# Kernel optimization log

Hardware: AMD Instinct MI355X
Metric: run time of the kernel (lower is better)

## Reference

```python
import jax, jax.numpy as jnp
import numpy as np
import math

B, S, HID = 1, 2048, 1024
NH, NKV = 16, 4
HD = HID // NH          # 64
GROUPS = NH // NKV      # 4
ROPE_BASE = 10000.0


def setup_inputs() -> dict:
    key = jax.random.key(0)
    ks = jax.random.split(key, 5)
    hidden_states = jax.random.normal(ks[0], (B, S, HID), dtype=jnp.float32)
    # additive causal mask: 0 on/below diagonal, -1e9 above
    causal = jnp.triu(jnp.full((S, S), -1e9, dtype=jnp.float32), k=1)
    attention_mask = causal[None, None, :, :]
    position_ids = jnp.arange(S, dtype=jnp.int32)[None, :]
    sc = 0.02
    Wq = jax.random.normal(ks[1], (NH * HD, HID), dtype=jnp.float32) * sc
    Wk = jax.random.normal(ks[2], (NKV * HD, HID), dtype=jnp.float32) * sc
    Wv = jax.random.normal(ks[3], (NKV * HD, HID), dtype=jnp.float32) * sc
    Wo = jax.random.normal(ks[4], (HID, NH * HD), dtype=jnp.float32) * sc
    return {"hidden_states": hidden_states, "attention_mask": attention_mask,
            "position_ids": position_ids, "Wq": Wq, "Wk": Wk, "Wv": Wv, "Wo": Wo}


def _rotate_half(x):
    x1, x2 = jnp.split(x, 2, axis=-1)
    return jnp.concatenate([-x2, x1], axis=-1)


def _rope_cos_sin(position_ids, dtype):
    # LlamaRotaryEmbedding: inv_freq over even dims, emb = [freqs, freqs]
    inv_freq = 1.0 / (ROPE_BASE ** (jnp.arange(0, HD, 2, dtype=jnp.float32) / HD))
    freqs = position_ids.astype(jnp.float32)[..., None] * inv_freq  # [B,S,HD/2]
    emb = jnp.concatenate([freqs, freqs], axis=-1)                  # [B,S,HD]
    return jnp.cos(emb).astype(dtype)[:, None], jnp.sin(emb).astype(dtype)[:, None]


def reference(hidden_states, attention_mask, position_ids, Wq, Wk, Wv, Wo):
    b, q_len, _ = hidden_states.shape
    # torch Linear: y = x @ W.T  (W is [out, in])
    q = jnp.einsum('bsh,oh->bso', hidden_states, Wq).reshape(b, q_len, NH, HD).transpose(0, 2, 1, 3)
    k = jnp.einsum('bsh,oh->bso', hidden_states, Wk).reshape(b, q_len, NKV, HD).transpose(0, 2, 1, 3)
    v = jnp.einsum('bsh,oh->bso', hidden_states, Wv).reshape(b, q_len, NKV, HD).transpose(0, 2, 1, 3)

    cos, sin = _rope_cos_sin(position_ids, q.dtype)  # [B,1,S,HD]
    q = q * cos + _rotate_half(q) * sin
    k = k * cos + _rotate_half(k) * sin

    # repeat_kv (GQA expansion)
    k = jnp.repeat(k, GROUPS, axis=1)  # [B,NH,S,HD]
    v = jnp.repeat(v, GROUPS, axis=1)

    scores = jnp.einsum('bhqd,bhkd->bhqk', q, k) / math.sqrt(HD)
    scores = scores + attention_mask
    attn = jax.nn.softmax(scores.astype(jnp.float32), axis=-1).astype(q.dtype)
    out = jnp.einsum('bhqk,bhkd->bhqd', attn, v)
    out = out.transpose(0, 2, 1, 3).reshape(b, q_len, NH * HD)
    return jnp.einsum('bso,ho->bsh', out, Wo)
```

## Files before the change

kernel.cpp:

```cpp
#include <hip/hip_runtime.h>
#include <hip/hip_bf16.h>
#include <math.h>

#define S_LEN 2048
#define HIDN  1024
#define K_DIM 1024
#define NHEAD 16
#define NKVH  4
#define HD    64

typedef __bf16 bf16x8 __attribute__((ext_vector_type(8)));
typedef float  f32x4  __attribute__((ext_vector_type(4)));
typedef float  f32x16 __attribute__((ext_vector_type(16)));

static __device__ __forceinline__ unsigned short f2bf(float f) {
  union { float f; unsigned u; } v; v.f = f;
  unsigned u = v.u;
  u += 0x7fffu + ((u >> 16) & 1u);
  return (unsigned short)(u >> 16);
}

static __device__ __forceinline__ void gload_lds16(const unsigned short* g, unsigned short* l) {
  __builtin_amdgcn_global_load_lds((const __attribute__((address_space(1))) void*)g,
                                   (__attribute__((address_space(3))) void*)l, 16, 0, 0);
}

__global__ __launch_bounds__(256) void prep_kernel(const float* __restrict__ hs,
                                                   const float* __restrict__ Wq,
                                                   const float* __restrict__ Wk,
                                                   const float* __restrict__ Wv,
                                                   const float* __restrict__ Wo,
                                                   const int* __restrict__ pos,
                                                   unsigned short* __restrict__ hsb,
                                                   unsigned short* __restrict__ Wqkv,
                                                   unsigned short* __restrict__ Wob,
                                                   float2* __restrict__ cstab) {
  const int gid = blockIdx.x * 256 + threadIdx.x;
  if (gid < 1179648) {
    const float* src; unsigned short* dst; int i;
    if (gid < 524288)       { src = hs; dst = hsb;            i = gid; }
    else if (gid < 786432)  { src = Wq; dst = Wqkv;           i = gid - 524288; }
    else if (gid < 851968)  { src = Wk; dst = Wqkv + 1048576; i = gid - 786432; }
    else if (gid < 917504)  { src = Wv; dst = Wqkv + 1310720; i = gid - 851968; }
    else                    { src = Wo; dst = Wob;            i = gid - 917504; }
    float4 v = *(const float4*)(src + (size_t)i * 4);
    ushort4 u;
    u.x = f2bf(v.x); u.y = f2bf(v.y); u.z = f2bf(v.z); u.w = f2bf(v.w);
    *(ushort4*)(dst + (size_t)i * 4) = u;
  } else {
    int e = gid - 1179648;
    int s = e >> 5, ir = e & 31;
    float p = (float)pos[s];
    float ang = p * __expf(-(float)ir * 0.28782314f);
    float c, sn;
    sincosf(ang, &sn, &c);
    cstab[e] = make_float2(c, sn);
  }
}

template <bool ROPE>
__global__ __launch_bounds__(256, 2) void gemm_kernel(const unsigned short* __restrict__ A,
                                                      const unsigned short* __restrict__ B,
                                                      float* __restrict__ C,
                                                      const float2* __restrict__ cstab,
                                                      unsigned short* __restrict__ Qr,
                                                      unsigned short* __restrict__ Kr,
                                                      unsigned short* __restrict__ Vt) {
  __shared__ unsigned short As[2][64][64];
  __shared__ unsigned short Bs[2][128][64];
  const int m0 = blockIdx.x * 64, n0 = blockIdx.y * 128;
  const int t = threadIdx.x, w = t >> 6, lane = t & 63;
  const int lr = lane & 15, lg = lane >> 4;
  const int m_off = (w & 1) * 32, n_off = (w >> 1) * 64;
  const int rsub = lane >> 3;
  const int cole = ((lane & 7) * 8) ^ (rsub << 3);
  f32x4 acc[2][4] = {};

#define GSTAGE(b, kt) do {                                                     \
    _Pragma("unroll")                                                          \
    for (int c = 0; c < 2; ++c) {                                              \
      int ch = w * 2 + c;                                                      \
      gload_lds16(A + (size_t)(m0 + ch * 8 + rsub) * K_DIM + (kt) * 64 + cole, \
                  &As[b][0][0] + ch * 512);                                    \
    }                                                                          \
    _Pragma("unroll")                                                          \
    for (int c = 0; c < 4; ++c) {                                              \
      int ch = w * 4 + c;                                                      \
      gload_lds16(B + (size_t)(n0 + ch * 8 + rsub) * K_DIM + (kt) * 64 + cole, \
                  &Bs[b][0][0] + ch * 512);                                    \
    }                                                                          \
  } while (0)

  int cur = 0;
  GSTAGE(0, 0);
  for (int kt = 0; kt < 16; ++kt) {
    __syncthreads();
    if (kt + 1 < 16) GSTAGE(cur ^ 1, kt + 1);
#pragma unroll
    for (int kc = 0; kc < 2; ++kc) {
      bf16x8 af[2], bfg[4];
#pragma unroll
      for (int i = 0; i < 2; ++i) {
        int row = m_off + i * 16 + lr;
        af[i] = *(const bf16x8*)((const char*)&As[cur][0][0] + row * 128 +
                                 ((kc * 64 + lg * 16) ^ ((lr & 7) << 4)));
      }
#pragma unroll
      for (int jj = 0; jj < 4; ++jj) {
        int row = n_off + jj * 16 + lr;
        bfg[jj] = *(const bf16x8*)((const char*)&Bs[cur][0][0] + row * 128 +
                                   ((kc * 64 + lg * 16) ^ ((lr & 7) << 4)));
      }
#pragma unroll
      for (int i = 0; i < 2; ++i)
#pragma unroll
        for (int jj = 0; jj < 4; ++jj)
          acc[i][jj] = __builtin_amdgcn_mfma_f32_16x16x32_bf16(af[i], bfg[jj], acc[i][jj], 0, 0, 0);
    }
    cur ^= 1;
  }

  if constexpr (ROPE) {
    const int col64 = n0 + n_off;
    const int hh = col64 >> 6;
#pragma unroll
    for (int i = 0; i < 2; ++i) {
      if (hh < 20) {
#pragma unroll
        for (int r = 0; r < 4; ++r) {
          int srow = m0 + m_off + i * 16 + lg * 4 + r;
          unsigned short* dst = (hh < 16) ? (Qr + ((size_t)hh * S_LEN + srow) * HD)
                                          : (Kr + ((size_t)(hh - 16) * S_LEN + srow) * HD);
          float sc = (hh < 16) ? 0.125f : 1.0f;
#pragma unroll
          for (int jj = 0; jj < 2; ++jj) {
            int d0 = jj * 16 + lr;
            float2 cs = cstab[(size_t)srow * 32 + d0];
            float v0 = acc[i][jj][r] * sc, v1 = acc[i][jj + 2][r] * sc;
            dst[d0]      = f2bf(v0 * cs.x - v1 * cs.y);
            dst[d0 + 32] = f2bf(v1 * cs.x + v0 * cs.y);
          }
        }
      } else {
        const int khv = (col64 - 1280) >> 6;
        const int s_base = m0 + m_off + i * 16 + lg * 4;
#pragma unroll
        for (int jj = 0; jj < 4; ++jj) {
          int d = jj * 16 + lr;
          ushort4 u;
          u.x = f2bf(acc[i][jj][0]);
          u.y = f2bf(acc[i][jj][1]);
          u.z = f2bf(acc[i][jj][2]);
          u.w = f2bf(acc[i][jj][3]);
          *(ushort4*)(Vt + ((size_t)khv * HD + d) * S_LEN + s_base) = u;
        }
      }
    }
  } else {
#pragma unroll
    for (int i = 0; i < 2; ++i)
#pragma unroll
      for (int jj = 0; jj < 4; ++jj)
#pragma unroll
        for (int r = 0; r < 4; ++r)
          C[(size_t)(m0 + m_off + i * 16 + lg * 4 + r) * 1024 + n0 + n_off + jj * 16 + lr] =
              acc[i][jj][r];
  }
}

__global__ __launch_bounds__(256, 4) void attn_part(const unsigned short* __restrict__ Qr,
                                                    const unsigned short* __restrict__ Kr,
                                                    const unsigned short* __restrict__ Vt,
                                                    unsigned short* __restrict__ Ob,
                                                    float* __restrict__ Opart,
                                                    float* __restrict__ Mlpart) {
  __shared__ unsigned short Ks[2][64][64];
  __shared__ unsigned short Vs[2][64][64];
  const int bid = blockIdx.x;
  const int h = bid & 15;
  const int j = bid >> 4;
  int qt, ck;
  if (j < 16)      { qt = 15 - (j >> 2); ck = j & 3; }
  else if (j < 28) { int e = j - 16; int d3 = e / 3; qt = 11 - d3; ck = e - d3 * 3; }
  else if (j < 36) { int e = j - 28; qt = 7 - (e >> 1); ck = e & 1; }
  else             { qt = 39 - j; ck = 0; }
  const int kh = h >> 2;
  const int nkt_all = 2 * qt + 2;
  const int nch = (2 * qt + 9) >> 3;
  const int kt0 = ck * 8;
  const int kt1 = (kt0 + 8 < nkt_all) ? kt0 + 8 : nkt_all;

  const int t = threadIdx.x, w = t >> 6, lane = t & 63;
  const int ql = lane & 31, hi = lane >> 5;
  const int q = qt * 128 + w * 32 + ql;
  const int qwave_max = qt * 128 + w * 32 + 31;

  const unsigned short* Kh = Kr + (size_t)kh * S_LEN * HD;
  const unsigned short* Vh = Vt + (size_t)kh * HD * S_LEN;

  bf16x8 qf[4];
#pragma unroll
  for (int c = 0; c < 4; ++c)
    qf[c] = *(const bf16x8*)(Qr + ((size_t)h * S_LEN + q) * HD + c * 16 + hi * 8);

  const int rsub = lane >> 3;
  const int cole = ((lane & 7) * 8) ^ (rsub << 3);

#define ASTAGE(b, kt) do {                                                           \
    int k0s = (kt) * 64;                                                             \
    _Pragma("unroll")                                                                \
    for (int c = 0; c < 4; ++c) {                                                    \
      int ch = w * 4 + c;                                                            \
      if (ch < 8)                                                                    \
        gload_lds16(Kh + (size_t)(k0s + ch * 8 + rsub) * HD + cole,                  \
                    &Ks[b][0][0] + ch * 512);                                        \
      else                                                                           \
        gload_lds16(Vh + (size_t)((ch - 8) * 8 + rsub) * S_LEN + k0s + cole,         \
                    &Vs[b][0][0] + (ch - 8) * 512);                                  \
    }                                                                                \
  } while (0)

  float m_run = -1e30f, l_run = 0.f;
  f32x16 oacc[2] = {};
  int cur = 0;
  ASTAGE(0, kt0);
  for (int kt = kt0; kt < kt1; ++kt) {
    __syncthreads();
    if (kt + 1 < kt1) ASTAGE(cur ^ 1, kt + 1);
    const int k0 = kt * 64;
    if (k0 <= qwave_max) {
      f32x16 sacc[2] = {};
      __builtin_amdgcn_s_setprio(1);
#pragma unroll
      for (int tt = 0; tt < 2; ++tt)
#pragma unroll
        for (int c = 0; c < 4; ++c) {
          int row = tt * 32 + ql;
          bf16x8 kf = *(const bf16x8*)((const char*)&Ks[cur][0][0] + row * 128 +
                                       ((c * 32 + hi * 16) ^ ((ql & 7) << 4)));
          sacc[tt] = __builtin_amdgcn_mfma_f32_32x32x16_bf16(kf, qf[c], sacc[tt], 0, 0, 0);
        }
      __builtin_amdgcn_s_setprio(0);

      float p[32];
#pragma unroll
      for (int tt = 0; tt < 2; ++tt)
#pragma unroll
        for (int e = 0; e < 16; ++e) p[tt * 16 + e] = sacc[tt][e];

      if (k0 + 63 > q) {
#pragma unroll
        for (int tt = 0; tt < 2; ++tt)
#pragma unroll
          for (int e = 0; e < 16; ++e) {
            int kl = tt * 32 + (e & 3) + 8 * (e >> 2) + 4 * hi;
            if (k0 + kl > q) p[tt * 16 + e] = -1e30f;
          }
      }

      float mx = p[0];
#pragma unroll
      for (int e = 1; e < 32; ++e) mx = fmaxf(mx, p[e]);
      mx = fmaxf(mx, __shfl_xor(mx, 32));

      if (__any(mx > m_run + 8.0f)) {
        float mnew = fmaxf(m_run, mx);
        float f = __expf(m_run - mnew);
        l_run *= f;
        oacc[0] *= f; oacc[1] *= f;
        m_run = mnew;
      }

      float lsum = 0.f;
#pragma unroll
      for (int e = 0; e < 32; ++e) { p[e] = __expf(p[e] - m_run); lsum += p[e]; }
      lsum += __shfl_xor(lsum, 32);
      l_run += lsum;

      unsigned g[16];
#pragma unroll
      for (int i = 0; i < 16; ++i) {
        union { __hip_bfloat162 b; unsigned u; } cv;
        cv.b = __float22bfloat162_rn(make_float2(p[2 * i], p[2 * i + 1]));
        g[i] = cv.u;
      }
#pragma unroll
      for (int b4 = 0; b4 < 16; b4 += 8) {
        asm volatile("v_permlane32_swap_b32 %0, %1" : "+v"(g[b4 + 0]), "+v"(g[b4 + 2]));
        asm volatile("v_permlane32_swap_b32 %0, %1" : "+v"(g[b4 + 1]), "+v"(g[b4 + 3]));
        asm volatile("v_permlane32_swap_b32 %0, %1" : "+v"(g[b4 + 4]), "+v"(g[b4 + 6]));
        asm volatile("v_permlane32_swap_b32 %0, %1" : "+v"(g[b4 + 5]), "+v"(g[b4 + 7]));
      }

#pragma unroll
      for (int s = 0; s < 4; ++s) {
        union { bf16x8 v; unsigned u[4]; } pf;
        pf.u[0] = g[s * 4 + 0]; pf.u[1] = g[s * 4 + 1];
        pf.u[2] = g[s * 4 + 2]; pf.u[3] = g[s * 4 + 3];
        __builtin_amdgcn_s_setprio(1);
#pragma unroll
        for (int dt = 0; dt < 2; ++dt) {
          int row = dt * 32 + ql;
          bf16x8 vf = *(const bf16x8*)((const char*)&Vs[cur][0][0] + row * 128 +
                                       ((s * 32 + hi * 16) ^ ((ql & 7) << 4)));
          oacc[dt] = __builtin_amdgcn_mfma_f32_32x32x16_bf16(vf, pf.v, oacc[dt], 0, 0, 0);
        }
        __builtin_amdgcn_s_setprio(0);
      }
    }
    cur ^= 1;
  }

  if (nch == 1) {
    float inv = 1.f / l_run;
#pragma unroll
    for (int dt = 0; dt < 2; ++dt)
#pragma unroll
      for (int gg = 0; gg < 4; ++gg) {
        ushort4 u;
        u.x = f2bf(oacc[dt][gg * 4 + 0] * inv);
        u.y = f2bf(oacc[dt][gg * 4 + 1] * inv);
        u.z = f2bf(oacc[dt][gg * 4 + 2] * inv);
        u.w = f2bf(oacc[dt][gg * 4 + 3] * inv);
        int d0 = dt * 32 + 8 * gg + 4 * hi;
        *(ushort4*)(Ob + (size_t)q * HIDN + h * HD + d0) = u;
      }
  } else {
    const int slot = (h * 16 + qt) * 4 + ck;
    float* ob = Opart + (size_t)slot * 8192 + t * 32;
#pragma unroll
    for (int dt = 0; dt < 2; ++dt)
#pragma unroll
      for (int gg = 0; gg < 4; ++gg) {
        f32x4 v4;
        v4[0] = oacc[dt][gg * 4 + 0]; v4[1] = oacc[dt][gg * 4 + 1];
        v4[2] = oacc[dt][gg * 4 + 2]; v4[3] = oacc[dt][gg * 4 + 3];
        *(f32x4*)(ob + dt * 16 + gg * 4) = v4;
      }
    if (hi == 0)
      *(float2*)(Mlpart + ((size_t)slot * 128 + w * 32 + ql) * 2) = make_float2(m_run, l_run);
  }
}

__global__ __launch_bounds__(256) void attn_merge(const float* __restrict__ Opart,
                                                  const float* __restrict__ Mlpart,
                                                  unsigned short* __restrict__ Ob) {
  const int h = blockIdx.x & 15, qt = 4 + (blockIdx.x >> 4);
  const int nch = (2 * qt + 9) >> 3;
  const int slotb = (h * 16 + qt) * 4;
  const int t = threadIdx.x;
  const int ql = t & 31, hi = (t >> 5) & 1, w = t >> 6;
  const int q_l = w * 32 + ql;
  const int q = qt * 128 + q_l;

  float mc[4], lc[4], mstar = -1e30f;
#pragma unroll
  for (int c = 0; c < 4; ++c)
    if (c < nch) {
      float2 ml = *(const float2*)(Mlpart + ((size_t)(slotb + c) * 128 + q_l) * 2);
      mc[c] = ml.x; lc[c] = ml.y;
      mstar = fmaxf(mstar, ml.x);
    }
  float wgt[4], lsum = 0.f;
#pragma unroll
  for (int c = 0; c < 4; ++c)
    if (c < nch) { wgt[c] = __expf(mc[c] - mstar); lsum += wgt[c] * lc[c]; }
  const float inv = 1.f / lsum;

#pragma unroll
  for (int g = 0; g < 8; ++g) {
    f32x4 a = {};
#pragma unroll
    for (int c = 0; c < 4; ++c)
      if (c < nch) {
        f32x4 v = *(const f32x4*)(Opart + (size_t)(slotb + c) * 8192 + t * 32 + g * 4);
        a += v * wgt[c];
      }
    int dt = g >> 2, gg = g & 3;
    int d0 = dt * 32 + 8 * gg + 4 * hi;
    ushort4 u;
    u.x = f2bf(a[0] * inv); u.y = f2bf(a[1] * inv);
    u.z = f2bf(a[2] * inv); u.w = f2bf(a[3] * inv);
    *(ushort4*)(Ob + (size_t)q * HIDN + h * HD + d0) = u;
  }
}

extern "C" void kernel_launch(void* const* d_in, const int* in_sizes, int n_in,
                              void* d_out, int out_size, void* d_ws, size_t ws_size,
                              hipStream_t stream) {
  const float* hs = (const float*)d_in[0];
  const int* pos = (const int*)d_in[2];
  const float* Wq = (const float*)d_in[3];
  const float* Wk = (const float*)d_in[4];
  const float* Wv = (const float*)d_in[5];
  const float* Wo = (const float*)d_in[6];
  float* out = (float*)d_out;

  char* ws = (char*)d_ws;
  unsigned short* hsb   = (unsigned short*)(ws);
  unsigned short* Wqkv  = (unsigned short*)(ws + 4194304);
  unsigned short* Wob   = (unsigned short*)(ws + 7340032);
  float2*         cstab = (float2*)(ws + 9437184);
  unsigned short* Qr    = (unsigned short*)(ws + 10485760);
  unsigned short* Kr    = (unsigned short*)(ws + 14680064);
  unsigned short* Vt    = (unsigned short*)(ws + 16777216);
  unsigned short* Ob    = (unsigned short*)(ws + 17825792);
  float*          Opart = (float*)(ws + 22020096);
  float*          Mlpart= (float*)(ws + 55574528);

  dim3 blk(256);
  prep_kernel<<<4864, blk, 0, stream>>>(hs, Wq, Wk, Wv, Wo, pos, hsb, Wqkv, Wob, cstab);
  gemm_kernel<true><<<dim3(32, 12), blk, 0, stream>>>(hsb, Wqkv, nullptr, cstab, Qr, Kr, Vt);
  attn_part<<<640, blk, 0, stream>>>(Qr, Kr, Vt, Ob, Opart, Mlpart);
  attn_merge<<<192, blk, 0, stream>>>(Opart, Mlpart, Ob);
  gemm_kernel<false><<<dim3(32, 8), blk, 0, stream>>>(Ob, Wob, out, nullptr, nullptr, nullptr, nullptr);
}
```

Baseline: 86.21 us.

## Process two 32-query sets per wave in attention to reuse K/V tiles

Each wave of the attention kernel now handles 64 queries (two 32-row sets) instead of 32, so every K and V fragment read from LDS feeds two MFMAs. The query tile per block doubles to 256, which halves the attention grid, and the split-K chunk schedule, partial buffers and merge kernel are remapped to match. The cost is roughly double the register use for accumulators, reflected in lowering launch bounds to 2 blocks per CU, and fewer blocks overall, which may leave CUs underused.

Measured after the change: 99.15 us. +15.0%, slower.

```diff
diff --git a/kernel.cpp b/kernel.cpp
--- a/kernel.cpp
+++ b/kernel.cpp
@@ -168,7 +168,7 @@
   }
 }
 
-__global__ __launch_bounds__(256, 4) void attn_part(const unsigned short* __restrict__ Qr,
+__global__ __launch_bounds__(256, 2) void attn_part(const unsigned short* __restrict__ Qr,
                                                     const unsigned short* __restrict__ Kr,
                                                     const unsigned short* __restrict__ Vt,
                                                     unsigned short* __restrict__ Ob,
@@ -180,28 +180,35 @@
   const int h = bid & 15;
   const int j = bid >> 4;
   int qt, ck;
-  if (j < 16)      { qt = 15 - (j >> 2); ck = j & 3; }
-  else if (j < 28) { int e = j - 16; int d3 = e / 3; qt = 11 - d3; ck = e - d3 * 3; }
-  else if (j < 36) { int e = j - 28; qt = 7 - (e >> 1); ck = e & 1; }
-  else             { qt = 39 - j; ck = 0; }
+  if (j < 4)        { qt = 7; ck = j; }
+  else if (j < 8)   { qt = 6; ck = j - 4; }
+  else if (j < 11)  { qt = 5; ck = j - 8; }
+  else if (j < 14)  { qt = 4; ck = j - 11; }
+  else if (j < 16)  { qt = 3; ck = j - 14; }
+  else if (j < 18)  { qt = 2; ck = j - 16; }
+  else if (j == 18) { qt = 1; ck = 0; }
+  else              { qt = 0; ck = 0; }
   const int kh = h >> 2;
-  const int nkt_all = 2 * qt + 2;
-  const int nch = (2 * qt + 9) >> 3;
+  const int nkt_all = 4 * qt + 4;
+  const int nch = (4 * qt + 11) >> 3;
   const int kt0 = ck * 8;
   const int kt1 = (kt0 + 8 < nkt_all) ? kt0 + 8 : nkt_all;
 
   const int t = threadIdx.x, w = t >> 6, lane = t & 63;
   const int ql = lane & 31, hi = lane >> 5;
-  const int q = qt * 128 + w * 32 + ql;
-  const int qwave_max = qt * 128 + w * 32 + 31;
+  const int qbase = qt * 256 + w * 64;
+  const int qA = qbase + ql, qB = qbase + 32 + ql;
+  const int qwave_max = qbase + 63;
 
   const unsigned short* Kh = Kr + (size_t)kh * S_LEN * HD;
   const unsigned short* Vh = Vt + (size_t)kh * HD * S_LEN;
 
-  bf16x8 qf[4];
-#pragma unroll
-  for (int c = 0; c < 4; ++c)
-    qf[c] = *(const bf16x8*)(Qr + ((size_t)h * S_LEN + q) * HD + c * 16 + hi * 8);
+  bf16x8 qfA[4], qfB[4];
+#pragma unroll
+  for (int c = 0; c < 4; ++c) {
+    qfA[c] = *(const bf16x8*)(Qr + ((size_t)h * S_LEN + qA) * HD + c * 16 + hi * 8);
+    qfB[c] = *(const bf16x8*)(Qr + ((size_t)h * S_LEN + qB) * HD + c * 16 + hi * 8);
+  }
 
   const int rsub = lane >> 3;
   const int cole = ((lane & 7) * 8) ^ (rsub << 3);
@@ -220,8 +227,54 @@
     }                                                                                \
   } while (0)
 
-  float m_run = -1e30f, l_run = 0.f;
-  f32x16 oacc[2] = {};
+#define SMAX(SACC, QV, MRUN, LRUN, OAC, G) do {                                      \
+    float p[32];                                                                     \
+    _Pragma("unroll")                                                                \
+    for (int tt = 0; tt < 2; ++tt)                                                   \
+      _Pragma("unroll")                                                              \
+      for (int e = 0; e < 16; ++e) p[tt * 16 + e] = SACC[tt][e];                     \
+    if (k0 + 63 > (QV)) {                                                            \
+      _Pragma("unroll")                                                              \
+      for (int tt = 0; tt < 2; ++tt)                                                 \
+        _Pragma("unroll")                                                            \
+        for (int e = 0; e < 16; ++e) {                                               \
+          int kl = tt * 32 + (e & 3) + 8 * (e >> 2) + 4 * hi;                        \
+          if (k0 + kl > (QV)) p[tt * 16 + e] = -1e30f;                               \
+        }                                                                            \
+    }                                                                                \
+    float mx = p[0];                                                                 \
+    _Pragma("unroll")                                                                \
+    for (int e = 1; e < 32; ++e) mx = fmaxf(mx, p[e]);                               \
+    mx = fmaxf(mx, __shfl_xor(mx, 32));                                              \
+    if (__any(mx > MRUN + 8.0f)) {                                                   \
+      float mnew = fmaxf(MRUN, mx);                                                  \
+      float f = __expf(MRUN - mnew);                                                 \
+      LRUN *= f;                                                                     \
+      OAC[0] *= f; OAC[1] *= f;                                                      \
+      MRUN = mnew;                                                                   \
+    }                                                                                \
+    float lsum = 0.f;                                                                \
+    _Pragma("unroll")                                                                \
+    for (int e = 0; e < 32; ++e) { p[e] = __expf(p[e] - MRUN); lsum += p[e]; }       \
+    lsum += __shfl_xor(lsum, 32);                                                    \
+    LRUN += lsum;                                                                    \
+    _Pragma("unroll")                                                                \
+    for (int i = 0; i < 16; ++i) {                                                   \
+      union { __hip_bfloat162 b; unsigned u; } cv;                                   \
+      cv.b = __float22bfloat162_rn(make_float2(p[2 * i], p[2 * i + 1]));             \
+      G[i] = cv.u;                                                                   \
+    }                                                                                \
+    _Pragma("unroll")                                                                \
+    for (int b4 = 0; b4 < 16; b4 += 8) {                                             \
+      asm volatile("v_permlane32_swap_b32 %0, %1" : "+v"(G[b4 + 0]), "+v"(G[b4 + 2]));\
+      asm volatile("v_permlane32_swap_b32 %0, %1" : "+v"(G[b4 + 1]), "+v"(G[b4 + 3]));\
+      asm volatile("v_permlane32_swap_b32 %0, %1" : "+v"(G[b4 + 4]), "+v"(G[b4 + 6]));\
+      asm volatile("v_permlane32_swap_b32 %0, %1" : "+v"(G[b4 + 5]), "+v"(G[b4 + 7]));\
+    }                                                                                \
+  } while (0)
+
+  float mA = -1e30f, lA = 0.f, mB = -1e30f, lB = 0.f;
+  f32x16 oA[2] = {}, oB[2] = {};
   int cur = 0;
   ASTAGE(0, kt0);
   for (int kt = kt0; kt < kt1; ++kt) {
@@ -229,7 +282,7 @@
     if (kt + 1 < kt1) ASTAGE(cur ^ 1, kt + 1);
     const int k0 = kt * 64;
     if (k0 <= qwave_max) {
-      f32x16 sacc[2] = {};
+      f32x16 sA[2] = {}, sB[2] = {};
       __builtin_amdgcn_s_setprio(1);
 #pragma unroll
       for (int tt = 0; tt < 2; ++tt)
@@ -238,72 +291,30 @@
           int row = tt * 32 + ql;
           bf16x8 kf = *(const bf16x8*)((const char*)&Ks[cur][0][0] + row * 128 +
                                        ((c * 32 + hi * 16) ^ ((ql & 7) << 4)));
-          sacc[tt] = __builtin_amdgcn_mfma_f32_32x32x16_bf16(kf, qf[c], sacc[tt], 0, 0, 0);
+          sA[tt] = __builtin_amdgcn_mfma_f32_32x32x16_bf16(kf, qfA[c], sA[tt], 0, 0, 0);
+          sB[tt] = __builtin_amdgcn_mfma_f32_32x32x16_bf16(kf, qfB[c], sB[tt], 0, 0, 0);
         }
       __builtin_amdgcn_s_setprio(0);
 
-      float p[32];
-#pragma unroll
-      for (int tt = 0; tt < 2; ++tt)
-#pragma unroll
-        for (int e = 0; e < 16; ++e) p[tt * 16 + e] = sacc[tt][e];
-
-      if (k0 + 63 > q) {
-#pragma unroll
-        for (int tt = 0; tt < 2; ++tt)
-#pragma unroll
-          for (int e = 0; e < 16; ++e) {
-            int kl = tt * 32 + (e & 3) + 8 * (e >> 2) + 4 * hi;
-            if (k0 + kl > q) p[tt * 16 + e] = -1e30f;
-          }
-      }
-
-      float mx = p[0];
-#pragma unroll
-      for (int e = 1; e < 32; ++e) mx = fmaxf(mx, p[e]);
-      mx = fmaxf(mx, __shfl_xor(mx, 32));
-
-      if (__any(mx > m_run + 8.0f)) {
-        float mnew = fmaxf(m_run, mx);
-        float f = __expf(m_run - mnew);
-        l_run *= f;
-        oacc[0] *= f; oacc[1] *= f;
-        m_run = mnew;
-      }
-
-      float lsum = 0.f;
-#pragma unroll
-      for (int e = 0; e < 32; ++e) { p[e] = __expf(p[e] - m_run); lsum += p[e]; }
-      lsum += __shfl_xor(lsum, 32);
-      l_run += lsum;
-
-      unsigned g[16];
-#pragma unroll
-      for (int i = 0; i < 16; ++i) {
-        union { __hip_bfloat162 b; unsigned u; } cv;
-        cv.b = __float22bfloat162_rn(make_float2(p[2 * i], p[2 * i + 1]));
-        g[i] = cv.u;
-      }
-#pragma unroll
-      for (int b4 = 0; b4 < 16; b4 += 8) {
-        asm volatile("v_permlane32_swap_b32 %0, %1" : "+v"(g[b4 + 0]), "+v"(g[b4 + 2]));
-        asm volatile("v_permlane32_swap_b32 %0, %1" : "+v"(g[b4 + 1]), "+v"(g[b4 + 3]));
-        asm volatile("v_permlane32_swap_b32 %0, %1" : "+v"(g[b4 + 4]), "+v"(g[b4 + 6]));
-        asm volatile("v_permlane32_swap_b32 %0, %1" : "+v"(g[b4 + 5]), "+v"(g[b4 + 7]));
-      }
+      unsigned gA[16], gB[16];
+      SMAX(sA, qA, mA, lA, oA, gA);
+      SMAX(sB, qB, mB, lB, oB, gB);
 
 #pragma unroll
       for (int s = 0; s < 4; ++s) {
-        union { bf16x8 v; unsigned u[4]; } pf;
-        pf.u[0] = g[s * 4 + 0]; pf.u[1] = g[s * 4 + 1];
-        pf.u[2] = g[s * 4 + 2]; pf.u[3] = g[s * 4 + 3];
+        union { bf16x8 v; unsigned u[4]; } pfA, pfB;
+        pfA.u[0] = gA[s * 4 + 0]; pfA.u[1] = gA[s * 4 + 1];
+        pfA.u[2] = gA[s * 4 + 2]; pfA.u[3] = gA[s * 4 + 3];
+        pfB.u[0] = gB[s * 4 + 0]; pfB.u[1] = gB[s * 4 + 1];
+        pfB.u[2] = gB[s * 4 + 2]; pfB.u[3] = gB[s * 4 + 3];
         __builtin_amdgcn_s_setprio(1);
 #pragma unroll
         for (int dt = 0; dt < 2; ++dt) {
           int row = dt * 32 + ql;
           bf16x8 vf = *(const bf16x8*)((const char*)&Vs[cur][0][0] + row * 128 +
                                        ((s * 32 + hi * 16) ^ ((ql & 7) << 4)));
-          oacc[dt] = __builtin_amdgcn_mfma_f32_32x32x16_bf16(vf, pf.v, oacc[dt], 0, 0, 0);
+          oA[dt] = __builtin_amdgcn_mfma_f32_32x32x16_bf16(vf, pfA.v, oA[dt], 0, 0, 0);
+          oB[dt] = __builtin_amdgcn_mfma_f32_32x32x16_bf16(vf, pfB.v, oB[dt], 0, 0, 0);
         }
         __builtin_amdgcn_s_setprio(0);
       }
@@ -312,76 +323,89 @@
   }
 
   if (nch == 1) {
-    float inv = 1.f / l_run;
+#define WRITE_O(OAC, LRUN, QV) do {                                                  \
+      float inv = 1.f / (LRUN);                                                      \
+      _Pragma("unroll")                                                              \
+      for (int dt = 0; dt < 2; ++dt)                                                 \
+        _Pragma("unroll")                                                            \
+        for (int gg = 0; gg < 4; ++gg) {                                             \
+          ushort4 u;                                                                 \
+          u.x = f2bf(OAC[dt][gg * 4 + 0] * inv);                                     \
+          u.y = f2bf(OAC[dt][gg * 4 + 1] * inv);                                     \
+          u.z = f2bf(OAC[dt][gg * 4 + 2] * inv);                                     \
+          u.w = f2bf(OAC[dt][gg * 4 + 3] * inv);                                     \
+          int d0 = dt * 32 + 8 * gg + 4 * hi;                                        \
+          *(ushort4*)(Ob + (size_t)(QV) * HIDN + h * HD + d0) = u;                   \
+        }                                                                            \
+    } while (0)
+    WRITE_O(oA, lA, qA);
+    WRITE_O(oB, lB, qB);
+  } else {
+    const int slot = (h * 8 + qt) * 4 + ck;
+    float* ob = Opart + (size_t)slot * 16384 + t * 64;
 #pragma unroll
     for (int dt = 0; dt < 2; ++dt)
 #pragma unroll
       for (int gg = 0; gg < 4; ++gg) {
-        ushort4 u;
-        u.x = f2bf(oacc[dt][gg * 4 + 0] * inv);
-        u.y = f2bf(oacc[dt][gg * 4 + 1] * inv);
-        u.z = f2bf(oacc[dt][gg * 4 + 2] * inv);
-        u.w = f2bf(oacc[dt][gg * 4 + 3] * inv);
-        int d0 = dt * 32 + 8 * gg + 4 * hi;
-        *(ushort4*)(Ob + (size_t)q * HIDN + h * HD + d0) = u;
-      }
-  } else {
-    const int slot = (h * 16 + qt) * 4 + ck;
-    float* ob = Opart + (size_t)slot * 8192 + t * 32;
-#pragma unroll
-    for (int dt = 0; dt < 2; ++dt)
-#pragma unroll
-      for (int gg = 0; gg < 4; ++gg) {
-        f32x4 v4;
-        v4[0] = oacc[dt][gg * 4 + 0]; v4[1] = oacc[dt][gg * 4 + 1];
-        v4[2] = oacc[dt][gg * 4 + 2]; v4[3] = oacc[dt][gg * 4 + 3];
-        *(f32x4*)(ob + dt * 16 + gg * 4) = v4;
-      }
-    if (hi == 0)
-      *(float2*)(Mlpart + ((size_t)slot * 128 + w * 32 + ql) * 2) = make_float2(m_run, l_run);
+        f32x4 a4, b4;
+        a4[0] = oA[dt][gg * 4 + 0]; a4[1] = oA[dt][gg * 4 + 1];
+        a4[2] = oA[dt][gg * 4 + 2]; a4[3] = oA[dt][gg * 4 + 3];
+        b4[0] = oB[dt][gg * 4 + 0]; b4[1] = oB[dt][gg * 4 + 1];
+        b4[2] = oB[dt][gg * 4 + 2]; b4[3] = oB[dt][gg * 4 + 3];
+        *(f32x4*)(ob + dt * 16 + gg * 4) = a4;
+        *(f32x4*)(ob + 32 + dt * 16 + gg * 4) = b4;
+      }
+    if (hi == 0) {
+      *(float2*)(Mlpart + ((size_t)slot * 256 + w * 64 + ql) * 2) = make_float2(mA, lA);
+      *(float2*)(Mlpart + ((size_t)slot * 256 + w * 64 + 32 + ql) * 2) = make_float2(mB, lB);
+    }
   }
 }
 
 __global__ __launch_bounds__(256) void attn_merge(const float* __restrict__ Opart,
                                                   const float* __restrict__ Mlpart,
                                                   unsigned short* __restrict__ Ob) {
-  const int h = blockIdx.x & 15, qt = 4 + (blockIdx.x >> 4);
-  const int nch = (2 * qt + 9) >> 3;
-  const int slotb = (h * 16 + qt) * 4;
-  const int t = threadIdx.x;
-  const int ql = t & 31, hi = (t >> 5) & 1, w = t >> 6;
-  const int q_l = w * 32 + ql;
-  const int q = qt * 128 + q_l;
-
-  float mc[4], lc[4], mstar = -1e30f;
-#pragma unroll
-  for (int c = 0; c < 4; ++c)
-    if (c < nch) {
-      float2 ml = *(const float2*)(Mlpart + ((size_t)(slotb + c) * 128 + q_l) * 2);
-      mc[c] = ml.x; lc[c] = ml.y;
-      mstar = fmaxf(mstar, ml.x);
-    }
-  float wgt[4], lsum = 0.f;
-#pragma unroll
-  for (int c = 0; c < 4; ++c)
-    if (c < nch) { wgt[c] = __expf(mc[c] - mstar); lsum += wgt[c] * lc[c]; }
-  const float inv = 1.f / lsum;
-
-#pragma unroll
-  for (int g = 0; g < 8; ++g) {
-    f32x4 a = {};
+  const int h = blockIdx.x & 15, qt = 2 + (blockIdx.x >> 4);
+  const int nch = (4 * qt + 11) >> 3;
+  const int slotb = (h * 8 + qt) * 4;
+  const int t = threadIdx.x, w = t >> 6, lane = t & 63;
+  const int ql = lane & 31, hi = lane >> 5;
+
+#pragma unroll
+  for (int set = 0; set < 2; ++set) {
+    const int q_l = w * 64 + set * 32 + ql;
+    const int q = qt * 256 + q_l;
+    float mc[4], lc[4], mstar = -1e30f;
 #pragma unroll
     for (int c = 0; c < 4; ++c)
       if (c < nch) {
-        f32x4 v = *(const f32x4*)(Opart + (size_t)(slotb + c) * 8192 + t * 32 + g * 4);
-        a += v * wgt[c];
-      }
-    int dt = g >> 2, gg = g & 3;
-    int d0 = dt * 32 + 8 * gg + 4 * hi;
-    ushort4 u;
-    u.x = f2bf(a[0] * inv); u.y = f2bf(a[1] * inv);
-    u.z = f2bf(a[2] * inv); u.w = f2bf(a[3] * inv);
-    *(ushort4*)(Ob + (size_t)q * HIDN + h * HD + d0) = u;
+        float2 ml = *(const float2*)(Mlpart + ((size_t)(slotb + c) * 256 + q_l) * 2);
+        mc[c] = ml.x; lc[c] = ml.y;
+        mstar = fmaxf(mstar, ml.x);
+      }
+    float wgt[4], lsum = 0.f;
+#pragma unroll
+    for (int c = 0; c < 4; ++c)
+      if (c < nch) { wgt[c] = __expf(mc[c] - mstar); lsum += wgt[c] * lc[c]; }
+    const float inv = 1.f / lsum;
+
+#pragma unroll
+    for (int g = 0; g < 8; ++g) {
+      f32x4 a = {};
+#pragma unroll
+      for (int c = 0; c < 4; ++c)
+        if (c < nch) {
+          f32x4 v = *(const f32x4*)(Opart + (size_t)(slotb + c) * 16384 + t * 64 +
+                                    set * 32 + g * 4);
+          a += v * wgt[c];
+        }
+      int dt = g >> 2, gg = g & 3;
+      int d0 = dt * 32 + 8 * gg + 4 * hi;
+      ushort4 u;
+      u.x = f2bf(a[0] * inv); u.y = f2bf(a[1] * inv);
+      u.z = f2bf(a[2] * inv); u.w = f2bf(a[3] * inv);
+      *(ushort4*)(Ob + (size_t)q * HIDN + h * HD + d0) = u;
+    }
   }
 }
 
@@ -411,7 +435,7 @@
   dim3 blk(256);
   prep_kernel<<<4864, blk, 0, stream>>>(hs, Wq, Wk, Wv, Wo, pos, hsb, Wqkv, Wob, cstab);
   gemm_kernel<true><<<dim3(32, 12), blk, 0, stream>>>(hsb, Wqkv, nullptr, cstab, Qr, Kr, Vt);
-  attn_part<<<640, blk, 0, stream>>>(Qr, Kr, Vt, Ob, Opart, Mlpart);
-  attn_merge<<<192, blk, 0, stream>>>(Opart, Mlpart, Ob);
+  attn_part<<<320, blk, 0, stream>>>(Qr, Kr, Vt, Ob, Opart, Mlpart);
+  attn_merge<<<96, blk, 0, stream>>>(Opart, Mlpart, Ob);
   gemm_kernel<false><<<dim3(32, 8), blk, 0, stream>>>(Ob, Wob, out, nullptr, nullptr, nullptr, nullptr);
 }
```

## Fuse split-KV merge into attention kernel via last-block atomic counter

Applied to the files above, without the earlier changes.

Removes the separate attn_merge launch. Each split-KV block of attn_part now increments a per-(head, q-tile) counter after writing its partials, and the last block to finish does the softmax-rescaled merge into Ob. This saves one kernel launch and its gap, but adds a hipMemsetAsync, threadfences and an atomic, and the merge work now runs serially on the tail block.

New measurement: 199.8 us. 132% more time.

```diff
diff --git a/kernel.cpp b/kernel.cpp
--- a/kernel.cpp
+++ b/kernel.cpp
@@ -173,9 +173,11 @@
                                                     const unsigned short* __restrict__ Vt,
                                                     unsigned short* __restrict__ Ob,
                                                     float* __restrict__ Opart,
-                                                    float* __restrict__ Mlpart) {
+                                                    float* __restrict__ Mlpart,
+                                                    unsigned* __restrict__ cnt) {
   __shared__ unsigned short Ks[2][64][64];
   __shared__ unsigned short Vs[2][64][64];
+  __shared__ unsigned s_old;
   const int bid = blockIdx.x;
   const int h = bid & 15;
   const int j = bid >> 4;
@@ -339,49 +341,43 @@
       }
     if (hi == 0)
       *(float2*)(Mlpart + ((size_t)slot * 128 + w * 32 + ql) * 2) = make_float2(m_run, l_run);
-  }
-}
-
-__global__ __launch_bounds__(256) void attn_merge(const float* __restrict__ Opart,
-                                                  const float* __restrict__ Mlpart,
-                                                  unsigned short* __restrict__ Ob) {
-  const int h = blockIdx.x & 15, qt = 4 + (blockIdx.x >> 4);
-  const int nch = (2 * qt + 9) >> 3;
-  const int slotb = (h * 16 + qt) * 4;
-  const int t = threadIdx.x;
-  const int ql = t & 31, hi = (t >> 5) & 1, w = t >> 6;
-  const int q_l = w * 32 + ql;
-  const int q = qt * 128 + q_l;
-
-  float mc[4], lc[4], mstar = -1e30f;
-#pragma unroll
-  for (int c = 0; c < 4; ++c)
-    if (c < nch) {
-      float2 ml = *(const float2*)(Mlpart + ((size_t)(slotb + c) * 128 + q_l) * 2);
-      mc[c] = ml.x; lc[c] = ml.y;
-      mstar = fmaxf(mstar, ml.x);
+
+    __threadfence();
+    __syncthreads();
+    if (t == 0) s_old = atomicAdd(&cnt[h * 16 + qt], 1u);
+    __syncthreads();
+    if (s_old == (unsigned)(nch - 1)) {
+      __threadfence();
+      const int slotb = (h * 16 + qt) * 4;
+      const int mql = t & 31, mhi = (t >> 5) & 1, mw = t >> 6;
+      const int q_l = mw * 32 + mql;
+      const int qq = qt * 128 + q_l;
+      float mc[4], lc[4], mstar = -1e30f;
+      for (int c = 0; c < 4; ++c)
+        if (c < nch) {
+          float2 ml = *(const float2*)(Mlpart + ((size_t)(slotb + c) * 128 + q_l) * 2);
+          mc[c] = ml.x; lc[c] = ml.y;
+          mstar = fmaxf(mstar, ml.x);
+        }
+      float wgt[4], msum = 0.f;
+      for (int c = 0; c < 4; ++c)
+        if (c < nch) { wgt[c] = __expf(mc[c] - mstar); msum += wgt[c] * lc[c]; }
+      const float minv = 1.f / msum;
+      for (int g2 = 0; g2 < 8; ++g2) {
+        f32x4 a = {};
+        for (int c = 0; c < 4; ++c)
+          if (c < nch) {
+            f32x4 v = *(const f32x4*)(Opart + (size_t)(slotb + c) * 8192 + t * 32 + g2 * 4);
+            a += v * wgt[c];
+          }
+        int dt = g2 >> 2, gg = g2 & 3;
+        int d0 = dt * 32 + 8 * gg + 4 * mhi;
+        ushort4 u;
+        u.x = f2bf(a[0] * minv); u.y = f2bf(a[1] * minv);
+        u.z = f2bf(a[2] * minv); u.w = f2bf(a[3] * minv);
+        *(ushort4*)(Ob + (size_t)qq * HIDN + h * HD + d0) = u;
+      }
     }
-  float wgt[4], lsum = 0.f;
-#pragma unroll
-  for (int c = 0; c < 4; ++c)
-    if (c < nch) { wgt[c] = __expf(mc[c] - mstar); lsum += wgt[c] * lc[c]; }
-  const float inv = 1.f / lsum;
-
-#pragma unroll
-  for (int g = 0; g < 8; ++g) {
-    f32x4 a = {};
-#pragma unroll
-    for (int c = 0; c < 4; ++c)
-      if (c < nch) {
-        f32x4 v = *(const f32x4*)(Opart + (size_t)(slotb + c) * 8192 + t * 32 + g * 4);
-        a += v * wgt[c];
-      }
-    int dt = g >> 2, gg = g & 3;
-    int d0 = dt * 32 + 8 * gg + 4 * hi;
-    ushort4 u;
-    u.x = f2bf(a[0] * inv); u.y = f2bf(a[1] * inv);
-    u.z = f2bf(a[2] * inv); u.w = f2bf(a[3] * inv);
-    *(ushort4*)(Ob + (size_t)q * HIDN + h * HD + d0) = u;
   }
 }
 
@@ -407,11 +403,13 @@
   unsigned short* Ob    = (unsigned short*)(ws + 17825792);
   float*          Opart = (float*)(ws + 22020096);
   float*          Mlpart= (float*)(ws + 55574528);
+  unsigned*       cnt   = (unsigned*)(ws + 56623104);
+
+  hipMemsetAsync(cnt, 0, 256 * sizeof(unsigned), stream);
 
   dim3 blk(256);
   prep_kernel<<<4864, blk, 0, stream>>>(hs, Wq, Wk, Wv, Wo, pos, hsb, Wqkv, Wob, cstab);
   gemm_kernel<true><<<dim3(32, 12), blk, 0, stream>>>(hsb, Wqkv, nullptr, cstab, Qr, Kr, Vt);
-  attn_part<<<640, blk, 0, stream>>>(Qr, Kr, Vt, Ob, Opart, Mlpart);
-  attn_merge<<<192, blk, 0, stream>>>(Opart, Mlpart, Ob);
+  attn_part<<<640, blk, 0, stream>>>(Qr, Kr, Vt, Ob, Opart, Mlpart, cnt);
   gemm_kernel<false><<<dim3(32, 8), blk, 0, stream>>>(Ob, Wob, out, nullptr, nullptr, nullptr, nullptr);
 }
```
